# Performance work log

Hardware: AMD Instinct MI355X
Metric: run time of the kernel (lower is better)

The kernel has to match this reference:

```python
import jax, jax.numpy as jnp
import numpy as np

N = 100000
SAMPLE = 25
FEAT = 128
HIDDEN = 128
CLASSES = 40


def setup_inputs() -> dict:
    key = jax.random.key(0)
    k_x, k_n, k_w1, k_w2, k_wl = jax.random.split(key, 5)
    X = jax.random.normal(k_x, (N, FEAT), dtype=jnp.float32)
    neighbors = jax.random.randint(k_n, (N, SAMPLE), 0, N, dtype=jnp.int32)
    # torch Linear weights are [out_features, in_features], xavier-uniform init
    def xavier(k, out_d, in_d):
        bound = float(np.sqrt(6.0 / (in_d + out_d)))
        return jax.random.uniform(k, (out_d, in_d), dtype=jnp.float32, minval=-bound, maxval=bound)
    W1 = xavier(k_w1, HIDDEN, FEAT)
    W2 = xavier(k_w2, HIDDEN, HIDDEN)
    Wlast = xavier(k_wl, CLASSES, HIDDEN)
    return {"X": X, "neighbors": neighbors, "W1": W1, "W2": W2, "Wlast": Wlast}


def reference(X, neighbors, W1, W2, Wlast):
    # forward: for each layer W: X = spmm(adj, X); X = X @ W.T; relu(X)
    # adj row i has sample_num entries of value 1/sample_num -> mean over sampled neighbors
    h = X
    for W in (W1, W2):
        agg = jnp.mean(h[neighbors], axis=1)          # [N, sample, d] -> [N, d]
        h = jax.nn.relu(jnp.einsum('nd,hd->nh', agg, W))
    return jnp.einsum('nh,ch->nc', h, Wlast)          # [N, class_num]
```

## Files before the change

### kernel.cpp

```cpp
#include <hip/hip_runtime.h>
#include <cstdint>
#include <cstddef>

typedef unsigned short u16;
typedef __bf16 bf16x8 __attribute__((ext_vector_type(8)));
typedef u16 u16x8 __attribute__((ext_vector_type(8)));
typedef float f32x4 __attribute__((ext_vector_type(4)));

#define N_NODES 100000
#define SAMPLE 25
#define FEAT 128
#define CLASSES 40

__device__ __forceinline__ float bf2f(u16 v) {
    return __uint_as_float(((unsigned)v) << 16);
}
__device__ __forceinline__ u16 f2bf(float f) {
    unsigned u = __float_as_uint(f);
    u += 0x7FFFu + ((u >> 16) & 1u);
    return (u16)(u >> 16);
}
__device__ __forceinline__ void split_bf(float x, u16& hi, u16& lo) {
    hi = f2bf(x);
    lo = f2bf(x - bf2f(hi));
}

__device__ __forceinline__ void split8(const float* ap, bf16x8& ah, bf16x8& al) {
    union { u16x8 u; bf16x8 b; } H, L;
    #pragma unroll
    for (int j = 0; j < 8; ++j) {
        u16 h, lo; split_bf(ap[j], h, lo);
        H.u[j] = h; L.u[j] = lo;
    }
    ah = H.b; al = L.b;
}

__device__ __forceinline__ f32x4 mfma_split(bf16x8 ah, bf16x8 al,
                                            bf16x8 bh, bf16x8 bl, f32x4 acc) {
    acc = __builtin_amdgcn_mfma_f32_16x16x32_bf16(ah, bh, acc, 0, 0, 0);
    acc = __builtin_amdgcn_mfma_f32_16x16x32_bf16(al, bh, acc, 0, 0, 0);
    acc = __builtin_amdgcn_mfma_f32_16x16x32_bf16(ah, bl, acc, 0, 0, 0);
    return acc;
}

__global__ __launch_bounds__(256) void prep_weights(
    const float* __restrict__ W1, const float* __restrict__ W2,
    const float* __restrict__ Wl,
    u16* __restrict__ w1h, u16* __restrict__ w1l,
    u16* __restrict__ w2h, u16* __restrict__ w2l,
    u16* __restrict__ wlh, u16* __restrict__ wll)
{
    const int i = blockIdx.x * 256 + threadIdx.x;
    const int stride = gridDim.x * 256;
    for (int j = i; j < FEAT * FEAT; j += stride) {
        split_bf(W1[j], w1h[j], w1l[j]);
        split_bf(W2[j], w2h[j], w2l[j]);
    }
    for (int j = i; j < CLASSES * FEAT; j += stride) {
        split_bf(Wl[j], wlh[j], wll[j]);
    }
}

#define NPB32 32
#define ZT_STRIDE 136

__global__ __launch_bounds__(128, 4) void k1_gemm(
    const float* __restrict__ X,
    const u16* __restrict__ w1h, const u16* __restrict__ w1l,
    u16* __restrict__ Z1)
{
    __shared__ u16 zt[NPB32][ZT_STRIDE];

    const int t = threadIdx.x;
    const int w  = t >> 6;
    const int l  = t & 63;
    const int lr = l & 15;
    const int lq = l >> 4;
    const int blockStart = blockIdx.x * NPB32;
    const float* Xrow = X + (size_t)(blockStart + w * 16 + lr) * FEAT;

    bf16x8 ah[4], al[4];
    #pragma unroll
    for (int k = 0; k < 4; ++k) {
        f32x4 x0 = *(const f32x4*)(Xrow + k * 32 + lq * 8);
        f32x4 x1 = *(const f32x4*)(Xrow + k * 32 + lq * 8 + 4);
        float tmp[8];
        #pragma unroll
        for (int j = 0; j < 4; ++j) { tmp[j] = x0[j]; tmp[4 + j] = x1[j]; }
        split8(tmp, ah[k], al[k]);
    }

    #pragma unroll
    for (int c = 0; c < 8; ++c) {
        f32x4 acc = {0.f, 0.f, 0.f, 0.f};
        #pragma unroll
        for (int k = 0; k < 4; ++k) {
            const size_t off = (size_t)(c * 16 + lr) * FEAT + k * 32 + lq * 8;
            bf16x8 bh = *(const bf16x8*)(w1h + off);
            bf16x8 bl = *(const bf16x8*)(w1l + off);
            acc = mfma_split(ah[k], al[k], bh, bl, acc);
        }
        #pragma unroll
        for (int r = 0; r < 4; ++r)
            zt[w * 16 + lq * 4 + r][c * 16 + lr] = f2bf(acc[r]);
    }
    __syncthreads();

    #pragma unroll
    for (int p = 0; p < 4; ++p) {
        const int idx = p * 128 + t;
        const int row = idx >> 4;
        const int col = (idx & 15) * 8;
        *(u16x8*)(Z1 + (size_t)(blockStart + row) * FEAT + col) =
            *(const u16x8*)&zt[row][col];
    }
}

__global__ __launch_bounds__(128, 3) void k2_hop(
    const u16* __restrict__ Zin, const int* __restrict__ nb,
    const u16* __restrict__ wh, const u16* __restrict__ wl,
    u16* __restrict__ Zout)
{
    __shared__ int nbs[NPB32 * SAMPLE];
    __shared__ float agg[NPB32][132];

    const int t = threadIdx.x;
    const int blockStart = blockIdx.x * NPB32;

    for (int i = t; i < NPB32 * SAMPLE; i += 128)
        nbs[i] = nb[blockStart * SAMPLE + i];
    __syncthreads();

    #pragma unroll 1
    for (int it = 0; it < 4; ++it) {
        const int item = t + it * 128;
        const int nl = item >> 4;
        const int fg = item & 15;
        const int* myn = &nbs[nl * SAMPLE];
        u16x8 buf[SAMPLE];
        #pragma unroll
        for (int s = 0; s < SAMPLE; ++s)
            buf[s] = *(const u16x8*)(Zin + ((size_t)myn[s] << 7) + fg * 8);
        float acc[8];
        #pragma unroll
        for (int j = 0; j < 8; ++j) acc[j] = 0.f;
        #pragma unroll
        for (int s = 0; s < SAMPLE; ++s) {
            #pragma unroll
            for (int j = 0; j < 8; ++j) acc[j] += bf2f(buf[s][j]);
        }
        #pragma unroll
        for (int j = 0; j < 8; ++j) {
            float m = acc[j] * (1.0f / SAMPLE);
            agg[nl][fg * 8 + j] = m > 0.f ? m : 0.f;
        }
    }
    __syncthreads();

    const int w  = t >> 6;
    const int l  = t & 63;
    const int lr = l & 15;
    const int lq = l >> 4;

    bf16x8 ah[4], al[4];
    #pragma unroll
    for (int k = 0; k < 4; ++k)
        split8(&agg[w * 16 + lr][k * 32 + lq * 8], ah[k], al[k]);
    __syncthreads();

    u16* zt = (u16*)agg;

    #pragma unroll
    for (int c = 0; c < 8; ++c) {
        f32x4 acc = {0.f, 0.f, 0.f, 0.f};
        #pragma unroll
        for (int k = 0; k < 4; ++k) {
            const size_t off = (size_t)(c * 16 + lr) * FEAT + k * 32 + lq * 8;
            bf16x8 bh = *(const bf16x8*)(wh + off);
            bf16x8 bl = *(const bf16x8*)(wl + off);
            acc = mfma_split(ah[k], al[k], bh, bl, acc);
        }
        #pragma unroll
        for (int r = 0; r < 4; ++r)
            zt[(size_t)(w * 16 + lq * 4 + r) * ZT_STRIDE + c * 16 + lr] = f2bf(acc[r]);
    }
    __syncthreads();

    #pragma unroll
    for (int p = 0; p < 4; ++p) {
        const int idx = p * 128 + t;
        const int row = idx >> 4;
        const int col = (idx & 15) * 8;
        *(u16x8*)(Zout + (size_t)(blockStart + row) * FEAT + col) =
            *(const u16x8*)&zt[(size_t)row * ZT_STRIDE + col];
    }
}

__global__ __launch_bounds__(128, 3) void k3_hop(
    const u16* __restrict__ Zin, const int* __restrict__ nb,
    const u16* __restrict__ wh, const u16* __restrict__ wl,
    float* __restrict__ out)
{
    __shared__ int nbs[NPB32 * SAMPLE];
    __shared__ float agg[NPB32][132];

    const int t = threadIdx.x;
    const int blockStart = blockIdx.x * NPB32;

    for (int i = t; i < NPB32 * SAMPLE; i += 128)
        nbs[i] = nb[blockStart * SAMPLE + i];
    __syncthreads();

    #pragma unroll 1
    for (int it = 0; it < 4; ++it) {
        const int item = t + it * 128;
        const int nl = item >> 4;
        const int fg = item & 15;
        const int* myn = &nbs[nl * SAMPLE];
        u16x8 buf[SAMPLE];
        #pragma unroll
        for (int s = 0; s < SAMPLE; ++s)
            buf[s] = *(const u16x8*)(Zin + ((size_t)myn[s] << 7) + fg * 8);
        float acc[8];
        #pragma unroll
        for (int j = 0; j < 8; ++j) acc[j] = 0.f;
        #pragma unroll
        for (int s = 0; s < SAMPLE; ++s) {
            #pragma unroll
            for (int j = 0; j < 8; ++j) acc[j] += bf2f(buf[s][j]);
        }
        #pragma unroll
        for (int j = 0; j < 8; ++j) {
            float m = acc[j] * (1.0f / SAMPLE);
            agg[nl][fg * 8 + j] = m > 0.f ? m : 0.f;
        }
    }
    __syncthreads();

    const int w  = t >> 6;
    const int l  = t & 63;
    const int lr = l & 15;
    const int lq = l >> 4;

    bf16x8 ah[4], al[4];
    #pragma unroll
    for (int k = 0; k < 4; ++k)
        split8(&agg[w * 16 + lr][k * 32 + lq * 8], ah[k], al[k]);

    #pragma unroll
    for (int c = 0; c < 3; ++c) {
        const int o = c * 16 + lr;
        f32x4 acc = {0.f, 0.f, 0.f, 0.f};
        #pragma unroll
        for (int k = 0; k < 4; ++k) {
            bf16x8 bh, bl;
            if (o < CLASSES) {
                const size_t off = (size_t)o * FEAT + k * 32 + lq * 8;
                bh = *(const bf16x8*)(wh + off);
                bl = *(const bf16x8*)(wl + off);
            } else {
                #pragma unroll
                for (int j = 0; j < 8; ++j) { bh[j] = (__bf16)0.f; bl[j] = (__bf16)0.f; }
            }
            acc = mfma_split(ah[k], al[k], bh, bl, acc);
        }
        if (o < CLASSES) {
            #pragma unroll
            for (int r = 0; r < 4; ++r) {
                const int node = blockStart + w * 16 + lq * 4 + r;
                out[(size_t)node * CLASSES + o] = acc[r];
            }
        }
    }
}

#define NPB 64
#define AGG_STRIDE 136

__global__ __launch_bounds__(256) void gnn_layer1(
    const float* __restrict__ X, const int* __restrict__ nb,
    const u16* __restrict__ w1h, const u16* __restrict__ w1l,
    u16* __restrict__ h1)
{
    __shared__ int nbs[NPB * SAMPLE];
    __shared__ u16 agg_h[NPB][AGG_STRIDE];
    __shared__ u16 agg_l[NPB][AGG_STRIDE];

    const int t = threadIdx.x;
    const int blockStart = blockIdx.x * NPB;

    for (int i = t; i < NPB * SAMPLE; i += 256) {
        int gi = blockStart * SAMPLE + i;
        if (gi >= N_NODES * SAMPLE) gi = N_NODES * SAMPLE - 1;
        nbs[i] = nb[gi];
    }
    __syncthreads();

    for (int item = t; item < NPB * 16; item += 256) {
        const int nl = item >> 4;
        const int fg = item & 15;
        float acc[8];
        #pragma unroll
        for (int j = 0; j < 8; ++j) acc[j] = 0.f;
        const int* myn = &nbs[nl * SAMPLE];
        for (int s = 0; s < SAMPLE; ++s) {
            const float4* p = (const float4*)(X + (size_t)myn[s] * FEAT + fg * 8);
            float4 a = p[0], b = p[1];
            acc[0] += a.x; acc[1] += a.y; acc[2] += a.z; acc[3] += a.w;
            acc[4] += b.x; acc[5] += b.y; acc[6] += b.z; acc[7] += b.w;
        }
        u16x8 oh, ol;
        #pragma unroll
        for (int j = 0; j < 8; ++j) {
            float m = acc[j] * (1.0f / SAMPLE);
            u16 h, lo; split_bf(m, h, lo);
            oh[j] = h; ol[j] = lo;
        }
        *(u16x8*)&agg_h[nl][fg * 8] = oh;
        *(u16x8*)&agg_l[nl][fg * 8] = ol;
    }
    __syncthreads();

    const int w  = t >> 6;
    const int l  = t & 63;
    const int lr = l & 15;
    const int lq = l >> 4;

    bf16x8 ah[4], al[4];
    #pragma unroll
    for (int k = 0; k < 4; ++k) {
        ah[k] = *(const bf16x8*)&agg_h[w * 16 + lr][k * 32 + lq * 8];
        al[k] = *(const bf16x8*)&agg_l[w * 16 + lr][k * 32 + lq * 8];
    }

    #pragma unroll
    for (int c = 0; c < 8; ++c) {
        f32x4 acc = {0.f, 0.f, 0.f, 0.f};
        #pragma unroll
        for (int k = 0; k < 4; ++k) {
            const size_t off = (size_t)(c * 16 + lr) * FEAT + k * 32 + lq * 8;
            bf16x8 bh = *(const bf16x8*)(w1h + off);
            bf16x8 bl = *(const bf16x8*)(w1l + off);
            acc = mfma_split(ah[k], al[k], bh, bl, acc);
        }
        #pragma unroll
        for (int r = 0; r < 4; ++r) {
            int node = blockStart + w * 16 + lq * 4 + r;
            if (node < N_NODES) {
                float v = acc[r] > 0.f ? acc[r] : 0.f;
                h1[(size_t)node * FEAT + c * 16 + lr] = f2bf(v);
            }
        }
    }
}

__global__ __launch_bounds__(256) void gnn_layer2_final(
    const u16* __restrict__ h1, const int* __restrict__ nb,
    const u16* __restrict__ w2h, const u16* __restrict__ w2l,
    const u16* __restrict__ wlh, const u16* __restrict__ wll,
    float* __restrict__ out)
{
    __shared__ int nbs[NPB * SAMPLE];
    __shared__ u16 agg_h[NPB][AGG_STRIDE];
    __shared__ u16 agg_l[NPB][AGG_STRIDE];

    const int t = threadIdx.x;
    const int blockStart = blockIdx.x * NPB;

    for (int i = t; i < NPB * SAMPLE; i += 256) {
        int gi = blockStart * SAMPLE + i;
        if (gi >= N_NODES * SAMPLE) gi = N_NODES * SAMPLE - 1;
        nbs[i] = nb[gi];
    }
    __syncthreads();

    for (int item = t; item < NPB * 16; item += 256) {
        const int nl = item >> 4;
        const int fg = item & 15;
        float acc[8];
        #pragma unroll
        for (int j = 0; j < 8; ++j) acc[j] = 0.f;
        const int* myn = &nbs[nl * SAMPLE];
        for (int s = 0; s < SAMPLE; ++s) {
            u16x8 v = *(const u16x8*)(h1 + (size_t)myn[s] * FEAT + fg * 8);
            #pragma unroll
            for (int j = 0; j < 8; ++j) acc[j] += bf2f(v[j]);
        }
        u16x8 oh, ol;
        #pragma unroll
        for (int j = 0; j < 8; ++j) {
            float m = acc[j] * (1.0f / SAMPLE);
            u16 h, lo; split_bf(m, h, lo);
            oh[j] = h; ol[j] = lo;
        }
        *(u16x8*)&agg_h[nl][fg * 8] = oh;
        *(u16x8*)&agg_l[nl][fg * 8] = ol;
    }
    __syncthreads();

    const int w  = t >> 6;
    const int l  = t & 63;
    const int lr = l & 15;
    const int lq = l >> 4;

    f32x4 hacc[8];
    {
        bf16x8 ah[4], al[4];
        #pragma unroll
        for (int k = 0; k < 4; ++k) {
            ah[k] = *(const bf16x8*)&agg_h[w * 16 + lr][k * 32 + lq * 8];
            al[k] = *(const bf16x8*)&agg_l[w * 16 + lr][k * 32 + lq * 8];
        }
        #pragma unroll
        for (int c = 0; c < 8; ++c) {
            f32x4 acc = {0.f, 0.f, 0.f, 0.f};
            #pragma unroll
            for (int k = 0; k < 4; ++k) {
                const size_t off = (size_t)(c * 16 + lr) * FEAT + k * 32 + lq * 8;
                bf16x8 bh = *(const bf16x8*)(w2h + off);
                bf16x8 bl = *(const bf16x8*)(w2l + off);
                acc = mfma_split(ah[k], al[k], bh, bl, acc);
            }
            hacc[c] = acc;
        }
    }
    __syncthreads();

    #pragma unroll
    for (int c = 0; c < 8; ++c) {
        #pragma unroll
        for (int r = 0; r < 4; ++r) {
            float v = hacc[c][r] > 0.f ? hacc[c][r] : 0.f;
            u16 h, l2; split_bf(v, h, l2);
            agg_h[w * 16 + lq * 4 + r][c * 16 + lr] = h;
            agg_l[w * 16 + lq * 4 + r][c * 16 + lr] = l2;
        }
    }
    __syncthreads();

    {
        bf16x8 ah[4], al[4];
        #pragma unroll
        for (int k = 0; k < 4; ++k) {
            ah[k] = *(const bf16x8*)&agg_h[w * 16 + lr][k * 32 + lq * 8];
            al[k] = *(const bf16x8*)&agg_l[w * 16 + lr][k * 32 + lq * 8];
        }
        #pragma unroll
        for (int c = 0; c < 3; ++c) {
            const int o = c * 16 + lr;
            f32x4 acc = {0.f, 0.f, 0.f, 0.f};
            #pragma unroll
            for (int k = 0; k < 4; ++k) {
                bf16x8 bh, bl;
                if (o < CLASSES) {
                    const size_t off = (size_t)o * FEAT + k * 32 + lq * 8;
                    bh = *(const bf16x8*)(wlh + off);
                    bl = *(const bf16x8*)(wll + off);
                } else {
                    #pragma unroll
                    for (int j = 0; j < 8; ++j) { bh[j] = (__bf16)0.f; bl[j] = (__bf16)0.f; }
                }
                acc = mfma_split(ah[k], al[k], bh, bl, acc);
            }
            if (o < CLASSES) {
                #pragma unroll
                for (int r = 0; r < 4; ++r) {
                    int node = blockStart + w * 16 + lq * 4 + r;
                    if (node < N_NODES) {
                        out[(size_t)node * CLASSES + o] = acc[r];
                    }
                }
            }
        }
    }
}

extern "C" void kernel_launch(void* const* d_in, const int* in_sizes, int n_in,
                              void* d_out, int out_size, void* d_ws, size_t ws_size,
                              hipStream_t stream) {
    const float* X  = (const float*)d_in[0];
    const int*   nb = (const int*)d_in[1];
    const float* W1 = (const float*)d_in[2];
    const float* W2 = (const float*)d_in[3];
    const float* Wl = (const float*)d_in[4];
    float* out = (float*)d_out;

    const size_t zelems = (size_t)N_NODES * FEAT;
    const size_t welems = 4 * (size_t)FEAT * FEAT + 2 * (size_t)CLASSES * FEAT;
    const size_t need_fast = (2 * zelems + welems) * sizeof(u16);

    if (ws_size >= need_fast) {
        u16* Z1  = (u16*)d_ws;
        u16* Z2  = Z1 + zelems;
        u16* w1h = Z2 + zelems;
        u16* w1l = w1h + FEAT * FEAT;
        u16* w2h = w1l + FEAT * FEAT;
        u16* w2l = w2h + FEAT * FEAT;
        u16* wlh = w2l + FEAT * FEAT;
        u16* wll = wlh + CLASSES * FEAT;

        prep_weights<<<64, 256, 0, stream>>>(W1, W2, Wl, w1h, w1l, w2h, w2l, wlh, wll);
        const int blocks = N_NODES / NPB32;
        k1_gemm<<<blocks, 128, 0, stream>>>(X, w1h, w1l, Z1);
        k2_hop<<<blocks, 128, 0, stream>>>(Z1, nb, w2h, w2l, Z2);
        k3_hop<<<blocks, 128, 0, stream>>>(Z2, nb, wlh, wll, out);
    } else {
        u16* h1  = (u16*)d_ws;
        u16* w1h = h1 + zelems;
        u16* w1l = w1h + FEAT * FEAT;
        u16* w2h = w1l + FEAT * FEAT;
        u16* w2l = w2h + FEAT * FEAT;
        u16* wlh = w2l + FEAT * FEAT;
        u16* wll = wlh + CLASSES * FEAT;

        prep_weights<<<64, 256, 0, stream>>>(W1, W2, Wl, w1h, w1l, w2h, w2l, wlh, wll);
        const int blocks = (N_NODES + NPB - 1) / NPB;
        gnn_layer1<<<blocks, 256, 0, stream>>>(X, nb, w1h, w1l, h1);
        gnn_layer2_final<<<blocks, 256, 0, stream>>>(h1, nb, w2h, w2l, wlh, wll, out);
    }
}
```

Baseline: 329.4 us.

## Pipeline neighbor gathers through LDS with async global_load_lds double buffering

Rewrites the neighbor-aggregation phase of both hop kernels. Each wave now streams rows directly into a double-buffered LDS slot with global_load_lds and manual waitcnt control, and accumulates in registers laid out to match the MFMA A-operand fragment. This removes the 25-deep register buffer and the separate agg shared array plus one barrier, and raises occupancy to 4 blocks per CU. The cost is reliance on hand-tuned vmcnt/lgkmcnt sequencing and a fixed LDS layout, where any mismatch would cause races.

```diff
diff --git a/kernel.cpp b/kernel.cpp
--- a/kernel.cpp
+++ b/kernel.cpp
@@ -41,6 +41,13 @@
     acc = __builtin_amdgcn_mfma_f32_16x16x32_bf16(al, bh, acc, 0, 0, 0);
     acc = __builtin_amdgcn_mfma_f32_16x16x32_bf16(ah, bl, acc, 0, 0, 0);
     return acc;
+}
+
+__device__ __forceinline__ void gload_lds16(const void* g, void* l) {
+    __builtin_amdgcn_global_load_lds(
+        (const __attribute__((address_space(1))) unsigned int*)g,
+        (__attribute__((address_space(3))) unsigned int*)l,
+        16, 0, 0);
 }
 
 __global__ __launch_bounds__(256) void prep_weights(
@@ -62,14 +69,13 @@
 }
 
 #define NPB32 32
-#define ZT_STRIDE 136
 
 __global__ __launch_bounds__(128, 4) void k1_gemm(
     const float* __restrict__ X,
     const u16* __restrict__ w1h, const u16* __restrict__ w1l,
     u16* __restrict__ Z1)
 {
-    __shared__ u16 zt[NPB32][ZT_STRIDE];
+    __shared__ u16 zt[NPB32][136];
 
     const int t = threadIdx.x;
     const int w  = t >> 6;
@@ -116,73 +122,104 @@
     }
 }
 
-__global__ __launch_bounds__(128, 3) void k2_hop(
+#define SLOT_BYTES   4224
+#define GROUP_STRIDE 1056
+#define WAVE_BYTES   8448
+
+__global__ __launch_bounds__(128, 4) void k2_hop(
     const u16* __restrict__ Zin, const int* __restrict__ nb,
     const u16* __restrict__ wh, const u16* __restrict__ wl,
     u16* __restrict__ Zout)
 {
+    __shared__ __align__(16) char slots[2 * WAVE_BYTES];
     __shared__ int nbs[NPB32 * SAMPLE];
-    __shared__ float agg[NPB32][132];
 
     const int t = threadIdx.x;
-    const int blockStart = blockIdx.x * NPB32;
-
-    for (int i = t; i < NPB32 * SAMPLE; i += 128)
-        nbs[i] = nb[blockStart * SAMPLE + i];
-    __syncthreads();
-
-    #pragma unroll 1
-    for (int it = 0; it < 4; ++it) {
-        const int item = t + it * 128;
-        const int nl = item >> 4;
-        const int fg = item & 15;
-        const int* myn = &nbs[nl * SAMPLE];
-        u16x8 buf[SAMPLE];
-        #pragma unroll
-        for (int s = 0; s < SAMPLE; ++s)
-            buf[s] = *(const u16x8*)(Zin + ((size_t)myn[s] << 7) + fg * 8);
-        float acc[8];
-        #pragma unroll
-        for (int j = 0; j < 8; ++j) acc[j] = 0.f;
-        #pragma unroll
-        for (int s = 0; s < SAMPLE; ++s) {
-            #pragma unroll
-            for (int j = 0; j < 8; ++j) acc[j] += bf2f(buf[s][j]);
-        }
-        #pragma unroll
-        for (int j = 0; j < 8; ++j) {
-            float m = acc[j] * (1.0f / SAMPLE);
-            agg[nl][fg * 8 + j] = m > 0.f ? m : 0.f;
-        }
-    }
-    __syncthreads();
-
     const int w  = t >> 6;
     const int l  = t & 63;
     const int lr = l & 15;
     const int lq = l >> 4;
+    const int blockStart = blockIdx.x * NPB32;
+
+    for (int i = t; i < NPB32 * SAMPLE; i += 128)
+        nbs[i] = nb[blockStart * SAMPLE + i];
+    __syncthreads();
+
+    char* base = slots + w * WAVE_BYTES;
+    const int srow = lq;
+    const int schk = lr;
+    char* rb0 = base + (lr >> 2) * GROUP_STRIDE + (lr & 3) * 256;
+
+    #define STAGE(s, slot)                                                    \
+        {                                                                     \
+            _Pragma("unroll")                                                 \
+            for (int g = 0; g < 4; ++g) {                                     \
+                const int nbrow = nbs[(w * 16 + g * 4 + srow) * SAMPLE + (s)];\
+                const u16* src = Zin + ((size_t)nbrow << 7) + schk * 8;       \
+                gload_lds16(src, base + (slot) * SLOT_BYTES + g * GROUP_STRIDE);\
+            }                                                                 \
+        }
+
+    float acc[4][8];
+    #pragma unroll
+    for (int k = 0; k < 4; ++k)
+        #pragma unroll
+        for (int j = 0; j < 8; ++j) acc[k][j] = 0.f;
+
+    #define CONSUME(slot)                                                     \
+        {                                                                     \
+            const char* rb = rb0 + (slot) * SLOT_BYTES;                       \
+            _Pragma("unroll")                                                 \
+            for (int k = 0; k < 4; ++k) {                                     \
+                u16x8 v = *(const u16x8*)(rb + (4 * k + lq) * 16);            \
+                _Pragma("unroll")                                             \
+                for (int j = 0; j < 8; ++j) acc[k][j] += bf2f(v[j]);          \
+            }                                                                 \
+        }
+
+    STAGE(0, 0);
+    STAGE(1, 1);
+    #pragma unroll 1
+    for (int s = 0; s < SAMPLE - 2; ++s) {
+        asm volatile("s_waitcnt vmcnt(4)" ::: "memory");
+        CONSUME(s & 1);
+        asm volatile("s_waitcnt lgkmcnt(0)" ::: "memory");
+        __builtin_amdgcn_sched_barrier(0);
+        STAGE(s + 2, s & 1);
+    }
+    asm volatile("s_waitcnt vmcnt(4)" ::: "memory");
+    CONSUME(1);
+    asm volatile("s_waitcnt vmcnt(0)" ::: "memory");
+    CONSUME(0);
 
     bf16x8 ah[4], al[4];
     #pragma unroll
-    for (int k = 0; k < 4; ++k)
-        split8(&agg[w * 16 + lr][k * 32 + lq * 8], ah[k], al[k]);
-    __syncthreads();
-
-    u16* zt = (u16*)agg;
+    for (int k = 0; k < 4; ++k) {
+        float tmp[8];
+        #pragma unroll
+        for (int j = 0; j < 8; ++j) {
+            float m = acc[k][j] * (1.0f / SAMPLE);
+            tmp[j] = m > 0.f ? m : 0.f;
+        }
+        split8(tmp, ah[k], al[k]);
+    }
+    __syncthreads();
+
+    u16* zt = (u16*)slots;
 
     #pragma unroll
     for (int c = 0; c < 8; ++c) {
-        f32x4 acc = {0.f, 0.f, 0.f, 0.f};
+        f32x4 o = {0.f, 0.f, 0.f, 0.f};
         #pragma unroll
         for (int k = 0; k < 4; ++k) {
             const size_t off = (size_t)(c * 16 + lr) * FEAT + k * 32 + lq * 8;
             bf16x8 bh = *(const bf16x8*)(wh + off);
             bf16x8 bl = *(const bf16x8*)(wl + off);
-            acc = mfma_split(ah[k], al[k], bh, bl, acc);
+            o = mfma_split(ah[k], al[k], bh, bl, o);
         }
         #pragma unroll
         for (int r = 0; r < 4; ++r)
-            zt[(size_t)(w * 16 + lq * 4 + r) * ZT_STRIDE + c * 16 + lr] = f2bf(acc[r]);
+            zt[(size_t)(w * 16 + lq * 4 + r) * 136 + c * 16 + lr] = f2bf(o[r]);
     }
     __syncthreads();
 
@@ -192,65 +229,94 @@
         const int row = idx >> 4;
         const int col = (idx & 15) * 8;
         *(u16x8*)(Zout + (size_t)(blockStart + row) * FEAT + col) =
-            *(const u16x8*)&zt[(size_t)row * ZT_STRIDE + col];
-    }
-}
-
-__global__ __launch_bounds__(128, 3) void k3_hop(
+            *(const u16x8*)&zt[(size_t)row * 136 + col];
+    }
+    #undef STAGE
+    #undef CONSUME
+}
+
+__global__ __launch_bounds__(128, 4) void k3_hop(
     const u16* __restrict__ Zin, const int* __restrict__ nb,
     const u16* __restrict__ wh, const u16* __restrict__ wl,
     float* __restrict__ out)
 {
+    __shared__ __align__(16) char slots[2 * WAVE_BYTES];
     __shared__ int nbs[NPB32 * SAMPLE];
-    __shared__ float agg[NPB32][132];
 
     const int t = threadIdx.x;
-    const int blockStart = blockIdx.x * NPB32;
-
-    for (int i = t; i < NPB32 * SAMPLE; i += 128)
-        nbs[i] = nb[blockStart * SAMPLE + i];
-    __syncthreads();
-
-    #pragma unroll 1
-    for (int it = 0; it < 4; ++it) {
-        const int item = t + it * 128;
-        const int nl = item >> 4;
-        const int fg = item & 15;
-        const int* myn = &nbs[nl * SAMPLE];
-        u16x8 buf[SAMPLE];
-        #pragma unroll
-        for (int s = 0; s < SAMPLE; ++s)
-            buf[s] = *(const u16x8*)(Zin + ((size_t)myn[s] << 7) + fg * 8);
-        float acc[8];
-        #pragma unroll
-        for (int j = 0; j < 8; ++j) acc[j] = 0.f;
-        #pragma unroll
-        for (int s = 0; s < SAMPLE; ++s) {
-            #pragma unroll
-            for (int j = 0; j < 8; ++j) acc[j] += bf2f(buf[s][j]);
-        }
-        #pragma unroll
-        for (int j = 0; j < 8; ++j) {
-            float m = acc[j] * (1.0f / SAMPLE);
-            agg[nl][fg * 8 + j] = m > 0.f ? m : 0.f;
-        }
-    }
-    __syncthreads();
-
     const int w  = t >> 6;
     const int l  = t & 63;
     const int lr = l & 15;
     const int lq = l >> 4;
+    const int blockStart = blockIdx.x * NPB32;
+
+    for (int i = t; i < NPB32 * SAMPLE; i += 128)
+        nbs[i] = nb[blockStart * SAMPLE + i];
+    __syncthreads();
+
+    char* base = slots + w * WAVE_BYTES;
+    const int srow = lq;
+    const int schk = lr;
+    char* rb0 = base + (lr >> 2) * GROUP_STRIDE + (lr & 3) * 256;
+
+    #define STAGE(s, slot)                                                    \
+        {                                                                     \
+            _Pragma("unroll")                                                 \
+            for (int g = 0; g < 4; ++g) {                                     \
+                const int nbrow = nbs[(w * 16 + g * 4 + srow) * SAMPLE + (s)];\
+                const u16* src = Zin + ((size_t)nbrow << 7) + schk * 8;       \
+                gload_lds16(src, base + (slot) * SLOT_BYTES + g * GROUP_STRIDE);\
+            }                                                                 \
+        }
+
+    float acc[4][8];
+    #pragma unroll
+    for (int k = 0; k < 4; ++k)
+        #pragma unroll
+        for (int j = 0; j < 8; ++j) acc[k][j] = 0.f;
+
+    #define CONSUME(slot)                                                     \
+        {                                                                     \
+            const char* rb = rb0 + (slot) * SLOT_BYTES;                       \
+            _Pragma("unroll")                                                 \
+            for (int k = 0; k < 4; ++k) {                                     \
+                u16x8 v = *(const u16x8*)(rb + (4 * k + lq) * 16);            \
+                _Pragma("unroll")                                             \
+                for (int j = 0; j < 8; ++j) acc[k][j] += bf2f(v[j]);          \
+            }                                                                 \
+        }
+
+    STAGE(0, 0);
+    STAGE(1, 1);
+    #pragma unroll 1
+    for (int s = 0; s < SAMPLE - 2; ++s) {
+        asm volatile("s_waitcnt vmcnt(4)" ::: "memory");
+        CONSUME(s & 1);
+        asm volatile("s_waitcnt lgkmcnt(0)" ::: "memory");
+        __builtin_amdgcn_sched_barrier(0);
+        STAGE(s + 2, s & 1);
+    }
+    asm volatile("s_waitcnt vmcnt(4)" ::: "memory");
+    CONSUME(1);
+    asm volatile("s_waitcnt vmcnt(0)" ::: "memory");
+    CONSUME(0);
 
     bf16x8 ah[4], al[4];
     #pragma unroll
-    for (int k = 0; k < 4; ++k)
-        split8(&agg[w * 16 + lr][k * 32 + lq * 8], ah[k], al[k]);
+    for (int k = 0; k < 4; ++k) {
+        float tmp[8];
+        #pragma unroll
+        for (int j = 0; j < 8; ++j) {
+            float m = acc[k][j] * (1.0f / SAMPLE);
+            tmp[j] = m > 0.f ? m : 0.f;
+        }
+        split8(tmp, ah[k], al[k]);
+    }
 
     #pragma unroll
     for (int c = 0; c < 3; ++c) {
         const int o = c * 16 + lr;
-        f32x4 acc = {0.f, 0.f, 0.f, 0.f};
+        f32x4 acc2 = {0.f, 0.f, 0.f, 0.f};
         #pragma unroll
         for (int k = 0; k < 4; ++k) {
             bf16x8 bh, bl;
@@ -262,16 +328,18 @@
                 #pragma unroll
                 for (int j = 0; j < 8; ++j) { bh[j] = (__bf16)0.f; bl[j] = (__bf16)0.f; }
             }
-            acc = mfma_split(ah[k], al[k], bh, bl, acc);
+            acc2 = mfma_split(ah[k], al[k], bh, bl, acc2);
         }
         if (o < CLASSES) {
             #pragma unroll
             for (int r = 0; r < 4; ++r) {
                 const int node = blockStart + w * 16 + lq * 4 + r;
-                out[(size_t)node * CLASSES + o] = acc[r];
+                out[(size_t)node * CLASSES + o] = acc2[r];
             }
         }
     }
+    #undef STAGE
+    #undef CONSUME
 }
 
 #define NPB 64
```

Result: slower. 358.4 us (+8.8%).

## Fuse first-layer GEMM into the hop kernel and pre-convert X to bf16

Applied to the files above, without the earlier changes.

The separate X@W1 GEMM kernel is removed. A widened prep kernel now converts X to bf16, and the first hop kernel gathers bf16 X rows, averages them, and applies W1, relu and W2 back to back. The mean and relu results stay in LDS as split hi/lo bf16 buffers. This saves one kernel launch and the pass that wrote the intermediate Z1. In exchange the gather works on rounded input features, the hop kernel does twice the MFMA work at lower occupancy, and the X conversion pass still streams all of X.

```diff
diff --git a/kernel.cpp b/kernel.cpp
--- a/kernel.cpp
+++ b/kernel.cpp
@@ -43,15 +43,27 @@
     return acc;
 }
 
-__global__ __launch_bounds__(256) void prep_weights(
+__global__ __launch_bounds__(256) void prep_all(
+    const float* __restrict__ X,
     const float* __restrict__ W1, const float* __restrict__ W2,
     const float* __restrict__ Wl,
+    u16* __restrict__ xb,
     u16* __restrict__ w1h, u16* __restrict__ w1l,
     u16* __restrict__ w2h, u16* __restrict__ w2l,
     u16* __restrict__ wlh, u16* __restrict__ wll)
 {
     const int i = blockIdx.x * 256 + threadIdx.x;
     const int stride = gridDim.x * 256;
+
+    const int nv = (N_NODES * FEAT) / 8;
+    for (int v = i; v < nv; v += stride) {
+        f32x4 a = *(const f32x4*)(X + (size_t)v * 8);
+        f32x4 b = *(const f32x4*)(X + (size_t)v * 8 + 4);
+        u16x8 o;
+        o[0] = f2bf(a[0]); o[1] = f2bf(a[1]); o[2] = f2bf(a[2]); o[3] = f2bf(a[3]);
+        o[4] = f2bf(b[0]); o[5] = f2bf(b[1]); o[6] = f2bf(b[2]); o[7] = f2bf(b[3]);
+        *(u16x8*)(xb + (size_t)v * 8) = o;
+    }
     for (int j = i; j < FEAT * FEAT; j += stride) {
         split_bf(W1[j], w1h[j], w1l[j]);
         split_bf(W2[j], w2h[j], w2l[j]);
@@ -64,65 +76,15 @@
 #define NPB32 32
 #define ZT_STRIDE 136
 
-__global__ __launch_bounds__(128, 4) void k1_gemm(
-    const float* __restrict__ X,
+__global__ __launch_bounds__(128, 2) void hopA(
+    const u16* __restrict__ Xb, const int* __restrict__ nb,
     const u16* __restrict__ w1h, const u16* __restrict__ w1l,
-    u16* __restrict__ Z1)
-{
-    __shared__ u16 zt[NPB32][ZT_STRIDE];
-
-    const int t = threadIdx.x;
-    const int w  = t >> 6;
-    const int l  = t & 63;
-    const int lr = l & 15;
-    const int lq = l >> 4;
-    const int blockStart = blockIdx.x * NPB32;
-    const float* Xrow = X + (size_t)(blockStart + w * 16 + lr) * FEAT;
-
-    bf16x8 ah[4], al[4];
-    #pragma unroll
-    for (int k = 0; k < 4; ++k) {
-        f32x4 x0 = *(const f32x4*)(Xrow + k * 32 + lq * 8);
-        f32x4 x1 = *(const f32x4*)(Xrow + k * 32 + lq * 8 + 4);
-        float tmp[8];
-        #pragma unroll
-        for (int j = 0; j < 4; ++j) { tmp[j] = x0[j]; tmp[4 + j] = x1[j]; }
-        split8(tmp, ah[k], al[k]);
-    }
-
-    #pragma unroll
-    for (int c = 0; c < 8; ++c) {
-        f32x4 acc = {0.f, 0.f, 0.f, 0.f};
-        #pragma unroll
-        for (int k = 0; k < 4; ++k) {
-            const size_t off = (size_t)(c * 16 + lr) * FEAT + k * 32 + lq * 8;
-            bf16x8 bh = *(const bf16x8*)(w1h + off);
-            bf16x8 bl = *(const bf16x8*)(w1l + off);
-            acc = mfma_split(ah[k], al[k], bh, bl, acc);
-        }
-        #pragma unroll
-        for (int r = 0; r < 4; ++r)
-            zt[w * 16 + lq * 4 + r][c * 16 + lr] = f2bf(acc[r]);
-    }
-    __syncthreads();
-
-    #pragma unroll
-    for (int p = 0; p < 4; ++p) {
-        const int idx = p * 128 + t;
-        const int row = idx >> 4;
-        const int col = (idx & 15) * 8;
-        *(u16x8*)(Z1 + (size_t)(blockStart + row) * FEAT + col) =
-            *(const u16x8*)&zt[row][col];
-    }
-}
-
-__global__ __launch_bounds__(128, 3) void k2_hop(
-    const u16* __restrict__ Zin, const int* __restrict__ nb,
-    const u16* __restrict__ wh, const u16* __restrict__ wl,
-    u16* __restrict__ Zout)
+    const u16* __restrict__ w2h, const u16* __restrict__ w2l,
+    u16* __restrict__ Z2)
 {
     __shared__ int nbs[NPB32 * SAMPLE];
-    __shared__ float agg[NPB32][132];
+    __shared__ u16 agg_h[NPB32][ZT_STRIDE];
+    __shared__ u16 agg_l[NPB32][ZT_STRIDE];
 
     const int t = threadIdx.x;
     const int blockStart = blockIdx.x * NPB32;
@@ -140,7 +102,7 @@
         u16x8 buf[SAMPLE];
         #pragma unroll
         for (int s = 0; s < SAMPLE; ++s)
-            buf[s] = *(const u16x8*)(Zin + ((size_t)myn[s] << 7) + fg * 8);
+            buf[s] = *(const u16x8*)(Xb + ((size_t)myn[s] << 7) + fg * 8);
         float acc[8];
         #pragma unroll
         for (int j = 0; j < 8; ++j) acc[j] = 0.f;
@@ -149,11 +111,15 @@
             #pragma unroll
             for (int j = 0; j < 8; ++j) acc[j] += bf2f(buf[s][j]);
         }
+        u16x8 oh, ol;
         #pragma unroll
         for (int j = 0; j < 8; ++j) {
-            float m = acc[j] * (1.0f / SAMPLE);
-            agg[nl][fg * 8 + j] = m > 0.f ? m : 0.f;
-        }
+            const float m = acc[j] * (1.0f / SAMPLE);
+            u16 h, lo; split_bf(m, h, lo);
+            oh[j] = h; ol[j] = lo;
+        }
+        *(u16x8*)&agg_h[nl][fg * 8] = oh;
+        *(u16x8*)&agg_l[nl][fg * 8] = ol;
     }
     __syncthreads();
 
@@ -162,27 +128,64 @@
     const int lr = l & 15;
     const int lq = l >> 4;
 
-    bf16x8 ah[4], al[4];
-    #pragma unroll
-    for (int k = 0; k < 4; ++k)
-        split8(&agg[w * 16 + lr][k * 32 + lq * 8], ah[k], al[k]);
-    __syncthreads();
-
-    u16* zt = (u16*)agg;
+    f32x4 hacc[8];
+    {
+        bf16x8 ah[4], al[4];
+        #pragma unroll
+        for (int k = 0; k < 4; ++k) {
+            ah[k] = *(const bf16x8*)&agg_h[w * 16 + lr][k * 32 + lq * 8];
+            al[k] = *(const bf16x8*)&agg_l[w * 16 + lr][k * 32 + lq * 8];
+        }
+        #pragma unroll
+        for (int c = 0; c < 8; ++c) {
+            f32x4 acc = {0.f, 0.f, 0.f, 0.f};
+            #pragma unroll
+            for (int k = 0; k < 4; ++k) {
+                const size_t off = (size_t)(c * 16 + lr) * FEAT + k * 32 + lq * 8;
+                bf16x8 bh = *(const bf16x8*)(w1h + off);
+                bf16x8 bl = *(const bf16x8*)(w1l + off);
+                acc = mfma_split(ah[k], al[k], bh, bl, acc);
+            }
+            hacc[c] = acc;
+        }
+    }
+    __syncthreads();
 
     #pragma unroll
     for (int c = 0; c < 8; ++c) {
-        f32x4 acc = {0.f, 0.f, 0.f, 0.f};
+        #pragma unroll
+        for (int r = 0; r < 4; ++r) {
+            float v = hacc[c][r] > 0.f ? hacc[c][r] : 0.f;
+            u16 h, l2; split_bf(v, h, l2);
+            agg_h[w * 16 + lq * 4 + r][c * 16 + lr] = h;
+            agg_l[w * 16 + lq * 4 + r][c * 16 + lr] = l2;
+        }
+    }
+    __syncthreads();
+
+    {
+        bf16x8 ah[4], al[4];
         #pragma unroll
         for (int k = 0; k < 4; ++k) {
-            const size_t off = (size_t)(c * 16 + lr) * FEAT + k * 32 + lq * 8;
-            bf16x8 bh = *(const bf16x8*)(wh + off);
-            bf16x8 bl = *(const bf16x8*)(wl + off);
-            acc = mfma_split(ah[k], al[k], bh, bl, acc);
-        }
-        #pragma unroll
-        for (int r = 0; r < 4; ++r)
-            zt[(size_t)(w * 16 + lq * 4 + r) * ZT_STRIDE + c * 16 + lr] = f2bf(acc[r]);
+            ah[k] = *(const bf16x8*)&agg_h[w * 16 + lr][k * 32 + lq * 8];
+            al[k] = *(const bf16x8*)&agg_l[w * 16 + lr][k * 32 + lq * 8];
+        }
+        __syncthreads();
+
+        #pragma unroll
+        for (int c = 0; c < 8; ++c) {
+            f32x4 acc = {0.f, 0.f, 0.f, 0.f};
+            #pragma unroll
+            for (int k = 0; k < 4; ++k) {
+                const size_t off = (size_t)(c * 16 + lr) * FEAT + k * 32 + lq * 8;
+                bf16x8 bh = *(const bf16x8*)(w2h + off);
+                bf16x8 bl = *(const bf16x8*)(w2l + off);
+                acc = mfma_split(ah[k], al[k], bh, bl, acc);
+            }
+            #pragma unroll
+            for (int r = 0; r < 4; ++r)
+                agg_h[w * 16 + lq * 4 + r][c * 16 + lr] = f2bf(acc[r]);
+        }
     }
     __syncthreads();
 
@@ -191,12 +194,12 @@
         const int idx = p * 128 + t;
         const int row = idx >> 4;
         const int col = (idx & 15) * 8;
-        *(u16x8*)(Zout + (size_t)(blockStart + row) * FEAT + col) =
-            *(const u16x8*)&zt[(size_t)row * ZT_STRIDE + col];
-    }
-}
-
-__global__ __launch_bounds__(128, 3) void k3_hop(
+        *(u16x8*)(Z2 + (size_t)(blockStart + row) * FEAT + col) =
+            *(const u16x8*)&agg_h[row][col];
+    }
+}
+
+__global__ __launch_bounds__(128, 3) void hopB(
     const u16* __restrict__ Zin, const int* __restrict__ nb,
     const u16* __restrict__ wh, const u16* __restrict__ wl,
     float* __restrict__ out)
@@ -490,8 +493,8 @@
     const size_t need_fast = (2 * zelems + welems) * sizeof(u16);
 
     if (ws_size >= need_fast) {
-        u16* Z1  = (u16*)d_ws;
-        u16* Z2  = Z1 + zelems;
+        u16* Xb  = (u16*)d_ws;
+        u16* Z2  = Xb + zelems;
         u16* w1h = Z2 + zelems;
         u16* w1l = w1h + FEAT * FEAT;
         u16* w2h = w1l + FEAT * FEAT;
@@ -499,11 +502,11 @@
         u16* wlh = w2l + FEAT * FEAT;
         u16* wll = wlh + CLASSES * FEAT;
 
-        prep_weights<<<64, 256, 0, stream>>>(W1, W2, Wl, w1h, w1l, w2h, w2l, wlh, wll);
+        prep_all<<<512, 256, 0, stream>>>(X, W1, W2, Wl, Xb,
+                                          w1h, w1l, w2h, w2l, wlh, wll);
         const int blocks = N_NODES / NPB32;
-        k1_gemm<<<blocks, 128, 0, stream>>>(X, w1h, w1l, Z1);
-        k2_hop<<<blocks, 128, 0, stream>>>(Z1, nb, w2h, w2l, Z2);
-        k3_hop<<<blocks, 128, 0, stream>>>(Z2, nb, wlh, wll, out);
+        hopA<<<blocks, 128, 0, stream>>>(Xb, nb, w1h, w1l, w2h, w2l, Z2);
+        hopB<<<blocks, 128, 0, stream>>>(Z2, nb, wlh, wll, out);
     } else {
         u16* h1  = (u16*)d_ws;
         u16* w1h = h1 + zelems;
@@ -513,7 +516,9 @@
         u16* wlh = w2l + FEAT * FEAT;
         u16* wll = wlh + CLASSES * FEAT;
 
-        prep_weights<<<64, 256, 0, stream>>>(W1, W2, Wl, w1h, w1l, w2h, w2l, wlh, wll);
+        prep_all<<<512, 256, 0, stream>>>(X, W1, W2, Wl,
+                                           h1,
+                                          w1h, w1l, w2h, w2l, wlh, wll);
         const int blocks = (N_NODES + NPB - 1) / NPB;
         gnn_layer1<<<blocks, 256, 0, stream>>>(X, nb, w1h, w1l, h1);
         gnn_layer2_final<<<blocks, 256, 0, stream>>>(h1, nb, w2h, w2l, wlh, wll, out);
```

Result: slower. 341.3 us (+3.6%).
